# Performance work log

Hardware: AMD Instinct MI355X
Metric: run time of the kernel (lower is better)

Reference implementation:

```python
import jax, jax.numpy as jnp
import numpy as np

N_DIM = 2  # number of trailing feature columns treated as coordinates


def setup_inputs() -> dict:
    key = jax.random.key(0)
    k1, k2, k3, k4 = jax.random.split(key, 4)
    B, N, F, O = 32, 1024, 64, 128
    x = jax.random.normal(k1, (B, N, F), dtype=jnp.float32)
    mask = (jax.random.uniform(k2, (B, N)) < 0.8).astype(jnp.float32)
    # A has shape ((F+1)*2 - 1, O) = (2F+1, O) per build()
    A = jax.random.normal(k3, ((F + 1) * 2 - 1, O), dtype=jnp.float32) * 0.05
    b = jax.random.normal(k4, (O,), dtype=jnp.float32) * 0.05
    return {"x": x, "mask": mask, "A": A, "b": b}


def reference(x, mask, A, b):
    # x: [B,N,F], mask: [B,N], A: [2F+1,O], b: [O]
    # TF tiles: a[b,i,j] = x[b,j]; b_t[b,i,j] = x[b,i]
    coords = x[:, :, -N_DIM:]                              # [B,N,d]
    # diff[b,i,j] = coords[b,j] - coords[b,i]  (ca - cb in TF)
    diff = coords[:, None, :, :] - coords[:, :, None, :]   # [B,N,N,d]
    dist = jnp.sum(diff * diff, axis=-1)                   # [B,N,N] (i,j)
    w = jnp.exp(-10.0 * dist)                              # [B,N,N]
    # TF: s[b,i,j,:] = concat(x[b,j], dist[b,i,j]) * w[b,i,j] * mask[b,j]
    #     ss[b,j]    = sum_i s[b,i,j]
    wsum = jnp.sum(w, axis=1)                              # [B,N] indexed by j
    dwsum = jnp.sum(dist * w, axis=1)                      # [B,N] indexed by j
    m = mask[..., None]                                    # [B,N,1]
    ss_feat = x * wsum[..., None] * m                      # [B,N,F]
    ss_dist = dwsum[..., None] * m                         # [B,N,1]
    ss = jnp.concatenate([ss_feat, ss_dist], axis=-1)      # [B,N,F+1]
    # subtract self term: xx = concat(x, 0)
    xx = jnp.concatenate([x, jnp.zeros_like(x[..., :1])], axis=-1)
    ss = ss - xx
    h = jnp.concatenate([x, ss], axis=-1)                  # [B,N,2F+1]
    out = (h @ A + b) * m                                  # [B,N,O]
    return out
```

## Files before the change

kernel.cpp:

```cpp
#include <hip/hip_runtime.h>
#include <hip/hip_bf16.h>

typedef __attribute__((ext_vector_type(8))) short bf16x8;
typedef __attribute__((ext_vector_type(4))) float f32x4;
typedef __attribute__((ext_vector_type(16))) float f32x16;

#define NN 1024
#define FF 64
#define OO 128

#define LOG2E    1.4426950408889634f
#define C20L     (20.0f * LOG2E)
#define C10L     (10.0f * LOG2E)
#define NEG_LN2_10 (-0.06931471805599453f)
#define BF1      ((short)0x3F80)

__device__ __forceinline__ short bfh(float f) {
    __hip_bfloat16 h = __float2bfloat16(f);
    return *reinterpret_cast<short*>(&h);
}
__device__ __forceinline__ float bf2f(short s) {
    union { unsigned u; float f; } v; v.u = ((unsigned)(unsigned short)s) << 16;
    return v.f;
}

__global__ __launch_bounds__(512) void gnn_fused_kernel(
    const float* __restrict__ x, const float* __restrict__ mask,
    const float* __restrict__ A, const float* __restrict__ bias,
    float* __restrict__ out)
{
    __shared__ __align__(16) short  ivec[NN * 8];
    __shared__ __align__(16) bf16x8 jlo[64], jhi[64];
    __shared__ __align__(16) bf16x8 cst;
    __shared__ float part_w[2][64], part_t[2][64];
    __shared__ __align__(16) float ws_s[64], dw_s[64];

    const int tid = threadIdx.x;
    const int w   = tid >> 6;
    const int l   = tid & 63;
    const int l16 = l & 15;
    const int lh  = l >> 4;

    const int bid = blockIdx.x;
    const int pos = bid >> 3;
    const int b   = (bid & 7) * 4 + (pos >> 4);
    const int jbase = (pos & 15) * 64;
    const int rowbase_g = b * NN + jbase;
    const float* xb = x + (size_t)b * NN * FF;

    #pragma unroll
    for (int q = 0; q < 2; ++q) {
        int p = tid + q * 512;
        float2 c2 = *(const float2*)(xb + (size_t)p * FF + (FF - 2));
        float vx = C20L * c2.x, vy = C20L * c2.y;
        float r2 = fmaf(c2.x, c2.x, c2.y * c2.y);
        float u  = -C10L * r2;
        short vxh = bfh(vx); short vxl = bfh(vx - bf2f(vxh));
        short vyh = bfh(vy); short vyl = bfh(vy - bf2f(vyh));
        short uh  = bfh(u);  short ul  = bfh(u  - bf2f(uh));
        bf16x8 iv = {vxh, vxl, vxh, vyh, vyl, vyh, uh, ul};
        *(bf16x8*)&ivec[p * 8] = iv;
        unsigned jloc = (unsigned)(p - jbase);
        if (jloc < 64u) {
            short xh = bfh(c2.x); short xl = bfh(c2.x - bf2f(xh));
            short yh = bfh(c2.y); short yl = bfh(c2.y - bf2f(yh));
            jlo[jloc] = (bf16x8){xh, xh, xl, yh, yh, yl, BF1, BF1};
            jhi[jloc] = (bf16x8){uh, ul, 0, 0, 0, 0, 0, 0};
        }
    }
    if (tid == 0) cst = (bf16x8){BF1, BF1, 0, 0, 0, 0, 0, 0};

    __syncthreads();

    const f32x4 Z4 = {0.f, 0.f, 0.f, 0.f};
    f32x4 acc[4][2][2];
    const int colbase = (w & 3) * 32;

    if (w >= 4) {
        const int jh_ = (w - 4) & 1;
        const int ih  = (w - 4) >> 1;
        const int j31 = l & 31;
        const bf16x8* bp = (l < 32) ? &jlo[32 * jh_ + j31] : &jhi[32 * jh_ + j31];
        bf16x8 Bj = *bp;
        const f32x16 Z = {0.f,0.f,0.f,0.f,0.f,0.f,0.f,0.f,
                          0.f,0.f,0.f,0.f,0.f,0.f,0.f,0.f};
        float aw0 = 0.f, aw1 = 0.f, at0 = 0.f, at1 = 0.f;
        __builtin_amdgcn_s_setprio(1);
        #pragma unroll
        for (int c = 0; c < 16; ++c) {
            const bf16x8* ap = (l < 32)
                ? (const bf16x8*)&ivec[(ih * 512 + c * 32 + j31) * 8]
                : &cst;
            bf16x8 Af = *ap;
            f32x16 S = __builtin_amdgcn_mfma_f32_32x32x16_bf16(Af, Bj, Z, 0, 0, 0);
            #pragma unroll
            for (int r = 0; r < 16; r += 2) {
                float p2a = S[r], p2b = S[r + 1];
                float wa = __builtin_amdgcn_exp2f(p2a);
                float wb = __builtin_amdgcn_exp2f(p2b);
                aw0 += wa;                 aw1 += wb;
                at0 = fmaf(p2a, wa, at0);  at1 = fmaf(p2b, wb, at1);
            }
        }
        __builtin_amdgcn_s_setprio(0);
        float aw = aw0 + aw1, at = at0 + at1;
        aw += __shfl_xor(aw, 32);
        at += __shfl_xor(at, 32);
        if (l < 32) {
            part_w[ih][32 * jh_ + j31] = aw;
            part_t[ih][32 * jh_ + j31] = at;
        }
    } else {
        bf16x8 Bh[2][2][2];
        #pragma unroll
        for (int cg = 0; cg < 2; ++cg)
            #pragma unroll
            for (int g = 0; g < 2; ++g)
                #pragma unroll
                for (int q = 0; q < 2; ++q) {
                    const float* ap = A + (size_t)(g * FF + 32 * q + 8 * lh) * OO
                                      + colbase + 16 * cg + l16;
                    #pragma unroll
                    for (int e = 0; e < 8; ++e)
                        Bh[cg][g][q][e] = bfh(ap[(size_t)e * OO]);
                }

        const float* xpb = x + (size_t)(rowbase_g + l16) * FF + 8 * lh;
        #pragma unroll
        for (int ms = 0; ms < 4; ++ms) {
            const float* _p = xpb + ms * 16 * FF;
            float4 v0 = *(const float4*)(_p);
            float4 v1 = *(const float4*)(_p + 4);
            float4 v2 = *(const float4*)(_p + 32);
            float4 v3 = *(const float4*)(_p + 36);
            float src[16] = {v0.x, v0.y, v0.z, v0.w, v1.x, v1.y, v1.z, v1.w,
                             v2.x, v2.y, v2.z, v2.w, v3.x, v3.y, v3.z, v3.w};
            bf16x8 Xh[2];
            #pragma unroll
            for (int q = 0; q < 2; ++q)
                #pragma unroll
                for (int e = 0; e < 8; ++e)
                    Xh[q][e] = bfh(src[q * 8 + e]);
            #pragma unroll
            for (int cg = 0; cg < 2; ++cg)
                #pragma unroll
                for (int g = 0; g < 2; ++g) {
                    acc[ms][cg][g] = __builtin_amdgcn_mfma_f32_16x16x32_bf16(
                        Xh[0], Bh[cg][g][0], Z4, 0, 0, 0);
                    acc[ms][cg][g] = __builtin_amdgcn_mfma_f32_16x16x32_bf16(
                        Xh[1], Bh[cg][g][1], acc[ms][cg][g], 0, 0, 0);
                }
        }
    }

    __syncthreads();
    if (tid < 64) {
        ws_s[tid] = part_w[0][tid] + part_w[1][tid];
        dw_s[tid] = (part_t[0][tid] + part_t[1][tid]) * NEG_LN2_10;
    }
    __syncthreads();

    if (w < 4) {
        float a2v[2], bbv[2];
        #pragma unroll
        for (int cg = 0; cg < 2; ++cg) {
            a2v[cg] = A[(size_t)(2 * FF) * OO + colbase + 16 * cg + l16];
            bbv[cg] = bias[colbase + 16 * cg + l16];
        }
        #pragma unroll
        for (int ms = 0; ms < 4; ++ms) {
            const int rl  = 16 * ms + 4 * lh;
            const int erg = rowbase_g + rl;
            float4 mk = *(const float4*)(mask + erg);
            float4 wv = *(const float4*)&ws_s[rl];
            float4 dv = *(const float4*)&dw_s[rl];
            float mks[4] = {mk.x, mk.y, mk.z, mk.w};
            float wvs[4] = {wv.x, wv.y, wv.z, wv.w};
            float dvs[4] = {dv.x, dv.y, dv.z, dv.w};
            #pragma unroll
            for (int r = 0; r < 4; ++r) {
                const int row = erg + r;
                const float m   = mks[r];
                const float s   = wvs[r] * m - 1.f;
                const float dwm = dvs[r] * m;
                #pragma unroll
                for (int cg = 0; cg < 2; ++cg) {
                    float val = acc[ms][cg][0][r] + s * acc[ms][cg][1][r]
                              + dwm * a2v[cg] + bbv[cg];
                    out[(size_t)row * OO + colbase + 16 * cg + l16] = val * m;
                }
            }
        }
    }
}

extern "C" void kernel_launch(void* const* d_in, const int* in_sizes, int n_in,
                              void* d_out, int out_size, void* d_ws, size_t ws_size,
                              hipStream_t stream)
{
    const float* x    = (const float*)d_in[0];
    const float* mask = (const float*)d_in[1];
    const float* A    = (const float*)d_in[2];
    const float* bias = (const float*)d_in[3];
    float* out = (float*)d_out;

    gnn_fused_kernel<<<dim3(512), dim3(512), 0, stream>>>(x, mask, A, bias, out);
}
```

Before: 16.61 us.

## Process two 64-row j tiles per block with overlapped pairwise and GEMM phases

Each block now handles 128 j rows in two 64-row steps, and the grid shrinks from 512 to 256 blocks. This halves how often the i-vector table is built in shared memory per batch. The GEMM waves compute tile t's projection, then wait at a barrier for the exp-sum waves' tile-t results, so the epilogue of one tile can overlap with the pairwise work of the next. The cost is fewer blocks on the device (256 on a large-CU GPU) and twice the serial exp work per block, which lengthens the critical path.

```diff
diff --git a/kernel.cpp b/kernel.cpp
--- a/kernel.cpp
+++ b/kernel.cpp
@@ -30,10 +30,10 @@
     float* __restrict__ out)
 {
     __shared__ __align__(16) short  ivec[NN * 8];
-    __shared__ __align__(16) bf16x8 jlo[64], jhi[64];
+    __shared__ __align__(16) bf16x8 jlo[128], jhi[128];
     __shared__ __align__(16) bf16x8 cst;
-    __shared__ float part_w[2][64], part_t[2][64];
-    __shared__ __align__(16) float ws_s[64], dw_s[64];
+    __shared__ __align__(16) float part_w[2][2][64];
+    __shared__ __align__(16) float part_t[2][2][64];
 
     const int tid = threadIdx.x;
     const int w   = tid >> 6;
@@ -42,9 +42,8 @@
     const int lh  = l >> 4;
 
     const int bid = blockIdx.x;
-    const int pos = bid >> 3;
-    const int b   = (bid & 7) * 4 + (pos >> 4);
-    const int jbase = (pos & 15) * 64;
+    const int b     = (bid & 7) * 4 + (bid >> 6);
+    const int jbase = ((bid >> 3) & 7) * 128;
     const int rowbase_g = b * NN + jbase;
     const float* xb = x + (size_t)b * NN * FF;
 
@@ -61,7 +60,7 @@
         bf16x8 iv = {vxh, vxl, vxh, vyh, vyl, vyh, uh, ul};
         *(bf16x8*)&ivec[p * 8] = iv;
         unsigned jloc = (unsigned)(p - jbase);
-        if (jloc < 64u) {
+        if (jloc < 128u) {
             short xh = bfh(c2.x); short xl = bfh(c2.x - bf2f(xh));
             short yh = bfh(c2.y); short yl = bfh(c2.y - bf2f(yh));
             jlo[jloc] = (bf16x8){xh, xh, xl, yh, yh, yl, BF1, BF1};
@@ -72,45 +71,49 @@
 
     __syncthreads();
 
-    const f32x4 Z4 = {0.f, 0.f, 0.f, 0.f};
-    f32x4 acc[4][2][2];
-    const int colbase = (w & 3) * 32;
-
     if (w >= 4) {
         const int jh_ = (w - 4) & 1;
         const int ih  = (w - 4) >> 1;
         const int j31 = l & 31;
-        const bf16x8* bp = (l < 32) ? &jlo[32 * jh_ + j31] : &jhi[32 * jh_ + j31];
-        bf16x8 Bj = *bp;
         const f32x16 Z = {0.f,0.f,0.f,0.f,0.f,0.f,0.f,0.f,
                           0.f,0.f,0.f,0.f,0.f,0.f,0.f,0.f};
-        float aw0 = 0.f, aw1 = 0.f, at0 = 0.f, at1 = 0.f;
-        __builtin_amdgcn_s_setprio(1);
-        #pragma unroll
-        for (int c = 0; c < 16; ++c) {
-            const bf16x8* ap = (l < 32)
-                ? (const bf16x8*)&ivec[(ih * 512 + c * 32 + j31) * 8]
-                : &cst;
-            bf16x8 Af = *ap;
-            f32x16 S = __builtin_amdgcn_mfma_f32_32x32x16_bf16(Af, Bj, Z, 0, 0, 0);
-            #pragma unroll
-            for (int r = 0; r < 16; r += 2) {
-                float p2a = S[r], p2b = S[r + 1];
-                float wa = __builtin_amdgcn_exp2f(p2a);
-                float wb = __builtin_amdgcn_exp2f(p2b);
-                aw0 += wa;                 aw1 += wb;
-                at0 = fmaf(p2a, wa, at0);  at1 = fmaf(p2b, wb, at1);
-            }
-        }
-        __builtin_amdgcn_s_setprio(0);
-        float aw = aw0 + aw1, at = at0 + at1;
-        aw += __shfl_xor(aw, 32);
-        at += __shfl_xor(at, 32);
-        if (l < 32) {
-            part_w[ih][32 * jh_ + j31] = aw;
-            part_t[ih][32 * jh_ + j31] = at;
+        for (int t = 0; t < 2; ++t) {
+            const int jj = t * 64 + 32 * jh_ + j31;
+            const bf16x8* bp = (l < 32) ? &jlo[jj] : &jhi[jj];
+            bf16x8 Bj = *bp;
+            float aw0 = 0.f, aw1 = 0.f, at0 = 0.f, at1 = 0.f;
+            __builtin_amdgcn_s_setprio(1);
+            #pragma unroll
+            for (int c = 0; c < 16; ++c) {
+                const bf16x8* ap = (l < 32)
+                    ? (const bf16x8*)&ivec[(ih * 512 + c * 32 + j31) * 8]
+                    : &cst;
+                bf16x8 Af = *ap;
+                f32x16 S = __builtin_amdgcn_mfma_f32_32x32x16_bf16(Af, Bj, Z, 0, 0, 0);
+                #pragma unroll
+                for (int r = 0; r < 16; r += 2) {
+                    float p2a = S[r], p2b = S[r + 1];
+                    float wa = __builtin_amdgcn_exp2f(p2a);
+                    float wb = __builtin_amdgcn_exp2f(p2b);
+                    aw0 += wa;                 aw1 += wb;
+                    at0 = fmaf(p2a, wa, at0);  at1 = fmaf(p2b, wb, at1);
+                }
+            }
+            __builtin_amdgcn_s_setprio(0);
+            float aw = aw0 + aw1, at = at0 + at1;
+            aw += __shfl_xor(aw, 32);
+            at += __shfl_xor(at, 32);
+            if (l < 32) {
+                part_w[t][ih][32 * jh_ + j31] = aw;
+                part_t[t][ih][32 * jh_ + j31] = at;
+            }
+            __syncthreads();
         }
     } else {
+        const int colbase = (w & 3) * 32;
+        const f32x4 Z4 = {0.f, 0.f, 0.f, 0.f};
+        f32x4 acc[4][2][2];
+
         bf16x8 Bh[2][2][2];
         #pragma unroll
         for (int cg = 0; cg < 2; ++cg)
@@ -124,70 +127,68 @@
                     for (int e = 0; e < 8; ++e)
                         Bh[cg][g][q][e] = bfh(ap[(size_t)e * OO]);
                 }
-
-        const float* xpb = x + (size_t)(rowbase_g + l16) * FF + 8 * lh;
-        #pragma unroll
-        for (int ms = 0; ms < 4; ++ms) {
-            const float* _p = xpb + ms * 16 * FF;
-            float4 v0 = *(const float4*)(_p);
-            float4 v1 = *(const float4*)(_p + 4);
-            float4 v2 = *(const float4*)(_p + 32);
-            float4 v3 = *(const float4*)(_p + 36);
-            float src[16] = {v0.x, v0.y, v0.z, v0.w, v1.x, v1.y, v1.z, v1.w,
-                             v2.x, v2.y, v2.z, v2.w, v3.x, v3.y, v3.z, v3.w};
-            bf16x8 Xh[2];
-            #pragma unroll
-            for (int q = 0; q < 2; ++q)
-                #pragma unroll
-                for (int e = 0; e < 8; ++e)
-                    Xh[q][e] = bfh(src[q * 8 + e]);
-            #pragma unroll
-            for (int cg = 0; cg < 2; ++cg)
-                #pragma unroll
-                for (int g = 0; g < 2; ++g) {
-                    acc[ms][cg][g] = __builtin_amdgcn_mfma_f32_16x16x32_bf16(
-                        Xh[0], Bh[cg][g][0], Z4, 0, 0, 0);
-                    acc[ms][cg][g] = __builtin_amdgcn_mfma_f32_16x16x32_bf16(
-                        Xh[1], Bh[cg][g][1], acc[ms][cg][g], 0, 0, 0);
-                }
-        }
-    }
-
-    __syncthreads();
-    if (tid < 64) {
-        ws_s[tid] = part_w[0][tid] + part_w[1][tid];
-        dw_s[tid] = (part_t[0][tid] + part_t[1][tid]) * NEG_LN2_10;
-    }
-    __syncthreads();
-
-    if (w < 4) {
         float a2v[2], bbv[2];
         #pragma unroll
         for (int cg = 0; cg < 2; ++cg) {
             a2v[cg] = A[(size_t)(2 * FF) * OO + colbase + 16 * cg + l16];
             bbv[cg] = bias[colbase + 16 * cg + l16];
         }
-        #pragma unroll
-        for (int ms = 0; ms < 4; ++ms) {
-            const int rl  = 16 * ms + 4 * lh;
-            const int erg = rowbase_g + rl;
-            float4 mk = *(const float4*)(mask + erg);
-            float4 wv = *(const float4*)&ws_s[rl];
-            float4 dv = *(const float4*)&dw_s[rl];
-            float mks[4] = {mk.x, mk.y, mk.z, mk.w};
-            float wvs[4] = {wv.x, wv.y, wv.z, wv.w};
-            float dvs[4] = {dv.x, dv.y, dv.z, dv.w};
-            #pragma unroll
-            for (int r = 0; r < 4; ++r) {
-                const int row = erg + r;
-                const float m   = mks[r];
-                const float s   = wvs[r] * m - 1.f;
-                const float dwm = dvs[r] * m;
-                #pragma unroll
-                for (int cg = 0; cg < 2; ++cg) {
-                    float val = acc[ms][cg][0][r] + s * acc[ms][cg][1][r]
-                              + dwm * a2v[cg] + bbv[cg];
-                    out[(size_t)row * OO + colbase + 16 * cg + l16] = val * m;
+
+        for (int t = 0; t < 2; ++t) {
+            const float* xpb = x + (size_t)(rowbase_g + t * 64 + l16) * FF + 8 * lh;
+            #pragma unroll
+            for (int ms = 0; ms < 4; ++ms) {
+                const float* _p = xpb + ms * 16 * FF;
+                float4 v0 = *(const float4*)(_p);
+                float4 v1 = *(const float4*)(_p + 4);
+                float4 v2 = *(const float4*)(_p + 32);
+                float4 v3 = *(const float4*)(_p + 36);
+                float src[16] = {v0.x, v0.y, v0.z, v0.w, v1.x, v1.y, v1.z, v1.w,
+                                 v2.x, v2.y, v2.z, v2.w, v3.x, v3.y, v3.z, v3.w};
+                bf16x8 Xh[2];
+                #pragma unroll
+                for (int q = 0; q < 2; ++q)
+                    #pragma unroll
+                    for (int e = 0; e < 8; ++e)
+                        Xh[q][e] = bfh(src[q * 8 + e]);
+                #pragma unroll
+                for (int cg = 0; cg < 2; ++cg)
+                    #pragma unroll
+                    for (int g = 0; g < 2; ++g) {
+                        acc[ms][cg][g] = __builtin_amdgcn_mfma_f32_16x16x32_bf16(
+                            Xh[0], Bh[cg][g][0], Z4, 0, 0, 0);
+                        acc[ms][cg][g] = __builtin_amdgcn_mfma_f32_16x16x32_bf16(
+                            Xh[1], Bh[cg][g][1], acc[ms][cg][g], 0, 0, 0);
+                    }
+            }
+
+            __syncthreads();
+
+            #pragma unroll
+            for (int ms = 0; ms < 4; ++ms) {
+                const int rl  = 16 * ms + 4 * lh;
+                const int erg = rowbase_g + t * 64 + rl;
+                float4 mk = *(const float4*)(mask + erg);
+                float4 w0 = *(const float4*)&part_w[t][0][rl];
+                float4 w1 = *(const float4*)&part_w[t][1][rl];
+                float4 t0 = *(const float4*)&part_t[t][0][rl];
+                float4 t1 = *(const float4*)&part_t[t][1][rl];
+                float mks[4] = {mk.x, mk.y, mk.z, mk.w};
+                float wvs[4] = {w0.x + w1.x, w0.y + w1.y, w0.z + w1.z, w0.w + w1.w};
+                float dvs[4] = {(t0.x + t1.x) * NEG_LN2_10, (t0.y + t1.y) * NEG_LN2_10,
+                                (t0.z + t1.z) * NEG_LN2_10, (t0.w + t1.w) * NEG_LN2_10};
+                #pragma unroll
+                for (int r = 0; r < 4; ++r) {
+                    const int row = erg + r;
+                    const float m   = mks[r];
+                    const float s   = wvs[r] * m - 1.f;
+                    const float dwm = dvs[r] * m;
+                    #pragma unroll
+                    for (int cg = 0; cg < 2; ++cg) {
+                        float val = acc[ms][cg][0][r] + s * acc[ms][cg][1][r]
+                                  + dwm * a2v[cg] + bbv[cg];
+                        out[(size_t)row * OO + colbase + 16 * cg + l16] = val * m;
+                    }
                 }
             }
         }
@@ -204,5 +205,5 @@
     const float* bias = (const float*)d_in[3];
     float* out = (float*)d_out;
 
-    gnn_fused_kernel<<<dim3(512), dim3(512), 0, stream>>>(x, mask, A, bias, out);
-}
+    gnn_fused_kernel<<<dim3(256), dim3(512), 0, stream>>>(x, mask, A, bias, out);
+}
```

Result: faster. 15.67 us, median of 2 (-5.7%).

## Split fused kernel into separate pairwise-reduction and GEMM kernels

Applied to the files above, without the earlier changes.

Splits the warp-specialized fused kernel into two launches. The first spends all 8 waves on the pairwise exp/dist reduction and writes per-row sums to a workspace. The second runs the projection GEMM and epilogue, reading those sums from global memory. This removes the imbalance where half the waves did the GEMM while the other half did the longer pairwise loop, at the cost of an extra kernel launch, a workspace round trip, and no overlap between the two phases.

```diff
diff --git a/kernel.cpp b/kernel.cpp
--- a/kernel.cpp
+++ b/kernel.cpp
@@ -24,29 +24,25 @@
     return v.f;
 }
 
-__global__ __launch_bounds__(512) void gnn_fused_kernel(
-    const float* __restrict__ x, const float* __restrict__ mask,
-    const float* __restrict__ A, const float* __restrict__ bias,
-    float* __restrict__ out)
+
+__global__ __launch_bounds__(512, 4) void pairwise_kernel(
+    const float* __restrict__ x,
+    float* __restrict__ gw, float* __restrict__ gt)
 {
     __shared__ __align__(16) short  ivec[NN * 8];
     __shared__ __align__(16) bf16x8 jlo[64], jhi[64];
     __shared__ __align__(16) bf16x8 cst;
-    __shared__ float part_w[2][64], part_t[2][64];
-    __shared__ __align__(16) float ws_s[64], dw_s[64];
+    __shared__ __align__(16) float part_w[2][4][32];
+    __shared__ __align__(16) float part_t[2][4][32];
 
     const int tid = threadIdx.x;
     const int w   = tid >> 6;
     const int l   = tid & 63;
-    const int l16 = l & 15;
-    const int lh  = l >> 4;
-
-    const int bid = blockIdx.x;
-    const int pos = bid >> 3;
-    const int b   = (bid & 7) * 4 + (pos >> 4);
-    const int jbase = (pos & 15) * 64;
-    const int rowbase_g = b * NN + jbase;
-    const float* xb = x + (size_t)b * NN * FF;
+
+    const int bid    = blockIdx.x;
+    const int b      = (bid & 7) * 4 + (bid >> 7);
+    const int jbase  = ((bid >> 3) & 15) * 64;
+    const float* xb  = x + (size_t)b * NN * FF;
 
     #pragma unroll
     for (int q = 0; q < 2; ++q) {
@@ -72,123 +68,139 @@
 
     __syncthreads();
 
+    const int jg  = w & 1;
+    const int iq  = w >> 1;
+    const int j31 = l & 31;
+    const bf16x8* bp = (l < 32) ? &jlo[32 * jg + j31] : &jhi[32 * jg + j31];
+    bf16x8 Bj = *bp;
+    const f32x16 Z = {0.f,0.f,0.f,0.f,0.f,0.f,0.f,0.f,
+                      0.f,0.f,0.f,0.f,0.f,0.f,0.f,0.f};
+    float aw0 = 0.f, aw1 = 0.f, at0 = 0.f, at1 = 0.f;
+    #pragma unroll
+    for (int c = 0; c < 8; ++c) {
+        const bf16x8* ap = (l < 32)
+            ? (const bf16x8*)&ivec[(iq * 256 + c * 32 + j31) * 8]
+            : &cst;
+        bf16x8 Af = *ap;
+        f32x16 S = __builtin_amdgcn_mfma_f32_32x32x16_bf16(Af, Bj, Z, 0, 0, 0);
+        #pragma unroll
+        for (int r = 0; r < 16; r += 2) {
+            float p2a = S[r], p2b = S[r + 1];
+            float wa = __builtin_amdgcn_exp2f(p2a);
+            float wb = __builtin_amdgcn_exp2f(p2b);
+            aw0 += wa;                 aw1 += wb;
+            at0 = fmaf(p2a, wa, at0);  at1 = fmaf(p2b, wb, at1);
+        }
+    }
+    float aw = aw0 + aw1, at = at0 + at1;
+    aw += __shfl_xor(aw, 32);
+    at += __shfl_xor(at, 32);
+    if (l < 32) {
+        part_w[jg][iq][j31] = aw;
+        part_t[jg][iq][j31] = at;
+    }
+    __syncthreads();
+
+    if (tid < 64) {
+        const int tg = tid >> 5, t31 = tid & 31;
+        float sw = (part_w[tg][0][t31] + part_w[tg][1][t31])
+                 + (part_w[tg][2][t31] + part_w[tg][3][t31]);
+        float st = (part_t[tg][0][t31] + part_t[tg][1][t31])
+                 + (part_t[tg][2][t31] + part_t[tg][3][t31]);
+        const int row = b * NN + jbase + tid;
+        gw[row] = sw;
+        gt[row] = st * NEG_LN2_10;
+    }
+}
+
+__global__ __launch_bounds__(256, 2) void gemm_kernel(
+    const float* __restrict__ x, const float* __restrict__ mask,
+    const float* __restrict__ A, const float* __restrict__ bias,
+    const float* __restrict__ gw, const float* __restrict__ gt,
+    float* __restrict__ out)
+{
+    const int tid = threadIdx.x;
+    const int w   = tid >> 6;
+    const int l   = tid & 63;
+    const int l16 = l & 15;
+    const int lh  = l >> 4;
+
+    const int bid = blockIdx.x;
+    const int b   = (bid & 7) * 4 + (bid >> 7);
+    const int rowbase_g = b * NN + ((bid >> 3) & 15) * 64;
+    const int colbase = w * 32;
+
     const f32x4 Z4 = {0.f, 0.f, 0.f, 0.f};
     f32x4 acc[4][2][2];
-    const int colbase = (w & 3) * 32;
-
-    if (w >= 4) {
-        const int jh_ = (w - 4) & 1;
-        const int ih  = (w - 4) >> 1;
-        const int j31 = l & 31;
-        const bf16x8* bp = (l < 32) ? &jlo[32 * jh_ + j31] : &jhi[32 * jh_ + j31];
-        bf16x8 Bj = *bp;
-        const f32x16 Z = {0.f,0.f,0.f,0.f,0.f,0.f,0.f,0.f,
-                          0.f,0.f,0.f,0.f,0.f,0.f,0.f,0.f};
-        float aw0 = 0.f, aw1 = 0.f, at0 = 0.f, at1 = 0.f;
-        __builtin_amdgcn_s_setprio(1);
-        #pragma unroll
-        for (int c = 0; c < 16; ++c) {
-            const bf16x8* ap = (l < 32)
-                ? (const bf16x8*)&ivec[(ih * 512 + c * 32 + j31) * 8]
-                : &cst;
-            bf16x8 Af = *ap;
-            f32x16 S = __builtin_amdgcn_mfma_f32_32x32x16_bf16(Af, Bj, Z, 0, 0, 0);
-            #pragma unroll
-            for (int r = 0; r < 16; r += 2) {
-                float p2a = S[r], p2b = S[r + 1];
-                float wa = __builtin_amdgcn_exp2f(p2a);
-                float wb = __builtin_amdgcn_exp2f(p2b);
-                aw0 += wa;                 aw1 += wb;
-                at0 = fmaf(p2a, wa, at0);  at1 = fmaf(p2b, wb, at1);
-            }
-        }
-        __builtin_amdgcn_s_setprio(0);
-        float aw = aw0 + aw1, at = at0 + at1;
-        aw += __shfl_xor(aw, 32);
-        at += __shfl_xor(at, 32);
-        if (l < 32) {
-            part_w[ih][32 * jh_ + j31] = aw;
-            part_t[ih][32 * jh_ + j31] = at;
-        }
-    } else {
-        bf16x8 Bh[2][2][2];
-        #pragma unroll
-        for (int cg = 0; cg < 2; ++cg)
-            #pragma unroll
-            for (int g = 0; g < 2; ++g)
-                #pragma unroll
-                for (int q = 0; q < 2; ++q) {
-                    const float* ap = A + (size_t)(g * FF + 32 * q + 8 * lh) * OO
-                                      + colbase + 16 * cg + l16;
-                    #pragma unroll
-                    for (int e = 0; e < 8; ++e)
-                        Bh[cg][g][q][e] = bfh(ap[(size_t)e * OO]);
-                }
-
-        const float* xpb = x + (size_t)(rowbase_g + l16) * FF + 8 * lh;
-        #pragma unroll
-        for (int ms = 0; ms < 4; ++ms) {
-            const float* _p = xpb + ms * 16 * FF;
-            float4 v0 = *(const float4*)(_p);
-            float4 v1 = *(const float4*)(_p + 4);
-            float4 v2 = *(const float4*)(_p + 32);
-            float4 v3 = *(const float4*)(_p + 36);
-            float src[16] = {v0.x, v0.y, v0.z, v0.w, v1.x, v1.y, v1.z, v1.w,
-                             v2.x, v2.y, v2.z, v2.w, v3.x, v3.y, v3.z, v3.w};
-            bf16x8 Xh[2];
-            #pragma unroll
-            for (int q = 0; q < 2; ++q)
+
+    bf16x8 Bh[2][2][2];
+    #pragma unroll
+    for (int cg = 0; cg < 2; ++cg)
+        #pragma unroll
+        for (int g = 0; g < 2; ++g)
+            #pragma unroll
+            for (int q = 0; q < 2; ++q) {
+                const float* ap = A + (size_t)(g * FF + 32 * q + 8 * lh) * OO
+                                  + colbase + 16 * cg + l16;
                 #pragma unroll
                 for (int e = 0; e < 8; ++e)
-                    Xh[q][e] = bfh(src[q * 8 + e]);
-            #pragma unroll
-            for (int cg = 0; cg < 2; ++cg)
-                #pragma unroll
-                for (int g = 0; g < 2; ++g) {
-                    acc[ms][cg][g] = __builtin_amdgcn_mfma_f32_16x16x32_bf16(
-                        Xh[0], Bh[cg][g][0], Z4, 0, 0, 0);
-                    acc[ms][cg][g] = __builtin_amdgcn_mfma_f32_16x16x32_bf16(
-                        Xh[1], Bh[cg][g][1], acc[ms][cg][g], 0, 0, 0);
-                }
-        }
-    }
-
-    __syncthreads();
-    if (tid < 64) {
-        ws_s[tid] = part_w[0][tid] + part_w[1][tid];
-        dw_s[tid] = (part_t[0][tid] + part_t[1][tid]) * NEG_LN2_10;
-    }
-    __syncthreads();
-
-    if (w < 4) {
-        float a2v[2], bbv[2];
-        #pragma unroll
-        for (int cg = 0; cg < 2; ++cg) {
-            a2v[cg] = A[(size_t)(2 * FF) * OO + colbase + 16 * cg + l16];
-            bbv[cg] = bias[colbase + 16 * cg + l16];
-        }
-        #pragma unroll
-        for (int ms = 0; ms < 4; ++ms) {
-            const int rl  = 16 * ms + 4 * lh;
-            const int erg = rowbase_g + rl;
-            float4 mk = *(const float4*)(mask + erg);
-            float4 wv = *(const float4*)&ws_s[rl];
-            float4 dv = *(const float4*)&dw_s[rl];
-            float mks[4] = {mk.x, mk.y, mk.z, mk.w};
-            float wvs[4] = {wv.x, wv.y, wv.z, wv.w};
-            float dvs[4] = {dv.x, dv.y, dv.z, dv.w};
-            #pragma unroll
-            for (int r = 0; r < 4; ++r) {
-                const int row = erg + r;
-                const float m   = mks[r];
-                const float s   = wvs[r] * m - 1.f;
-                const float dwm = dvs[r] * m;
-                #pragma unroll
-                for (int cg = 0; cg < 2; ++cg) {
-                    float val = acc[ms][cg][0][r] + s * acc[ms][cg][1][r]
-                              + dwm * a2v[cg] + bbv[cg];
-                    out[(size_t)row * OO + colbase + 16 * cg + l16] = val * m;
-                }
+                    Bh[cg][g][q][e] = bfh(ap[(size_t)e * OO]);
+            }
+    float a2v[2], bbv[2];
+    #pragma unroll
+    for (int cg = 0; cg < 2; ++cg) {
+        a2v[cg] = A[(size_t)(2 * FF) * OO + colbase + 16 * cg + l16];
+        bbv[cg] = bias[colbase + 16 * cg + l16];
+    }
+
+    const float* xpb = x + (size_t)(rowbase_g + l16) * FF + 8 * lh;
+    #pragma unroll
+    for (int ms = 0; ms < 4; ++ms) {
+        const float* _p = xpb + ms * 16 * FF;
+        float4 v0 = *(const float4*)(_p);
+        float4 v1 = *(const float4*)(_p + 4);
+        float4 v2 = *(const float4*)(_p + 32);
+        float4 v3 = *(const float4*)(_p + 36);
+        float src[16] = {v0.x, v0.y, v0.z, v0.w, v1.x, v1.y, v1.z, v1.w,
+                         v2.x, v2.y, v2.z, v2.w, v3.x, v3.y, v3.z, v3.w};
+        bf16x8 Xh[2];
+        #pragma unroll
+        for (int q = 0; q < 2; ++q)
+            #pragma unroll
+            for (int e = 0; e < 8; ++e)
+                Xh[q][e] = bfh(src[q * 8 + e]);
+        #pragma unroll
+        for (int cg = 0; cg < 2; ++cg)
+            #pragma unroll
+            for (int g = 0; g < 2; ++g) {
+                acc[ms][cg][g] = __builtin_amdgcn_mfma_f32_16x16x32_bf16(
+                    Xh[0], Bh[cg][g][0], Z4, 0, 0, 0);
+                acc[ms][cg][g] = __builtin_amdgcn_mfma_f32_16x16x32_bf16(
+                    Xh[1], Bh[cg][g][1], acc[ms][cg][g], 0, 0, 0);
+            }
+    }
+
+    #pragma unroll
+    for (int ms = 0; ms < 4; ++ms) {
+        const int rl  = 16 * ms + 4 * lh;
+        const int erg = rowbase_g + rl;
+        float4 mk = *(const float4*)(mask + erg);
+        float4 wv = *(const float4*)(gw + erg);
+        float4 dv = *(const float4*)(gt + erg);
+        float mks[4] = {mk.x, mk.y, mk.z, mk.w};
+        float wvs[4] = {wv.x, wv.y, wv.z, wv.w};
+        float dvs[4] = {dv.x, dv.y, dv.z, dv.w};
+        #pragma unroll
+        for (int r = 0; r < 4; ++r) {
+            const int row = erg + r;
+            const float m   = mks[r];
+            const float s   = wvs[r] * m - 1.f;
+            const float dwm = dvs[r] * m;
+            #pragma unroll
+            for (int cg = 0; cg < 2; ++cg) {
+                float val = acc[ms][cg][0][r] + s * acc[ms][cg][1][r]
+                          + dwm * a2v[cg] + bbv[cg];
+                out[(size_t)row * OO + colbase + 16 * cg + l16] = val * m;
             }
         }
     }
@@ -204,5 +216,9 @@
     const float* bias = (const float*)d_in[3];
     float* out = (float*)d_out;
 
-    gnn_fused_kernel<<<dim3(512), dim3(512), 0, stream>>>(x, mask, A, bias, out);
-}
+    float* gw = (float*)d_ws;
+    float* gt = gw + 32 * NN;
+
+    pairwise_kernel<<<dim3(512), dim3(512), 0, stream>>>(x, gw, gt);
+    gemm_kernel<<<dim3(512), dim3(256), 0, stream>>>(x, mask, A, bias, gw, gt, out);
+}
```

After: 21.87 us. 1.32x slower.
